# Kernel optimization log

Hardware: AMD Instinct MI355X
Metric: run time of the kernel (lower is better)

Reference implementation:

```python
import jax, jax.numpy as jnp
import numpy as np

DIM = 256
NUM_HEADS = 4
HEAD_DIM = DIM // NUM_HEADS
WINDOW_SIZES = [2, 4, 8, 16]
SCALE = HEAD_DIM ** -0.5


def setup_inputs() -> dict:
    key = jax.random.key(0)
    k1, k2, k3, k4 = jax.random.split(key, 4)
    B, C, H, W = 8, DIM, 128, 128
    x = jax.random.normal(k1, (B, C, H, W), dtype=jnp.float32)
    # 1x1 conv weights stored as [out, in]
    qkv_w = jax.random.normal(k2, (3 * DIM, DIM), dtype=jnp.float32) * (DIM ** -0.5)
    proj_w = jax.random.normal(k3, (DIM, DIM), dtype=jnp.float32) * (DIM ** -0.5)
    proj_b = jax.random.normal(k4, (DIM,), dtype=jnp.float32) * 0.01
    return {"x": x, "qkv_w": qkv_w, "proj_w": proj_w, "proj_b": proj_b}


def _window_attn(q, k, v, ws):
    # q,k,v: [B, H, W, hd] for one head; windowed self-attention of size ws
    B, H, W, hd = q.shape
    hg, wg = H // ws, W // ws

    def part(t):
        # [B,H,W,hd] -> [B, hg*wg, ws*ws, hd]
        t = t.reshape(B, hg, ws, wg, ws, hd).transpose(0, 1, 3, 2, 4, 5)
        return t.reshape(B, hg * wg, ws * ws, hd)

    qw, kw, vw = part(q), part(k), part(v)
    attn = jnp.einsum('bgqd,bgkd->bgqk', qw, kw) * SCALE
    attn = jax.nn.softmax(attn, axis=-1)
    out = jnp.einsum('bgqk,bgkd->bgqd', attn, vw)
    # reassemble: [B, hg, wg, ws, ws, hd] -> [B, H, W, hd]
    out = out.reshape(B, hg, wg, ws, ws, hd).transpose(0, 1, 3, 2, 4, 5)
    return out.reshape(B, H, W, hd)


def reference(x, qkv_w, proj_w, proj_b):
    B, C, H, W = x.shape
    # 1x1 conv qkv: [B, 3*dim, H, W] -> [3, B, nh, H, W, hd]
    qkv = jnp.einsum('bchw,oc->bohw', x, qkv_w)
    qkv = qkv.reshape(B, 3, NUM_HEADS, HEAD_DIM, H, W).transpose(1, 0, 2, 4, 5, 3)
    q, k, v = qkv[0], qkv[1], qkv[2]
    outs = []
    for i, ws in enumerate(WINDOW_SIZES):
        outs.append(_window_attn(q[:, i], k[:, i], v[:, i], ws))
    y = jnp.concatenate(outs, axis=-1)  # [B, H, W, dim]
    y = jnp.einsum('bhwc,oc->bhwo', y, proj_w) + proj_b
    y = y.transpose(0, 3, 1, 2)  # [B, dim, H, W]
    return y + x
```

## Files before the change

### kernel.cpp

```cpp
#include <hip/hip_runtime.h>
#include <hip/hip_bf16.h>
#include <cstddef>
#include <cstdint>

typedef unsigned short u16;
typedef unsigned int uint32;
typedef __attribute__((ext_vector_type(8))) short bf16x8;
typedef __attribute__((ext_vector_type(4))) float f32x4;

#define SPATIAL 16384
#define TOTAL_M 131072

__device__ __forceinline__ u16 f2b(float f) {
  __hip_bfloat16 h = __float2bfloat16(f);
  return *reinterpret_cast<u16*>(&h);
}
__device__ __forceinline__ uint32 pk2(float a, float b) {
  return (uint32)f2b(a) | ((uint32)f2b(b) << 16);
}
__device__ __forceinline__ float blo(uint32 u) {
  union { uint32 u; float f; } c; c.u = u << 16; return c.f;
}
__device__ __forceinline__ float bhi(uint32 u) {
  union { uint32 u; float f; } c; c.u = u & 0xffff0000u; return c.f;
}

__device__ __forceinline__ void gload_lds16(const u16* g, u16* l) {
  __builtin_amdgcn_global_load_lds(
      (const __attribute__((address_space(1))) void*)g,
      (__attribute__((address_space(3))) void*)l, 16, 0, 0);
}

template <int WS>
__device__ __forceinline__ size_t tok_base(int gw, int tt) {
  constexpr int WG = 128 / WS;
  constexpr int NWIN = WG * WG;
  int bb = gw / NWIN, rr = gw % NWIN;
  int gy = rr / WG, gx = rr % WG;
  int yy = gy * WS + tt / WS, xx = gx * WS + tt % WS;
  return (((size_t)bb * 128 + yy) * 128 + xx) * 768;
}

__global__ __launch_bounds__(256) void prep(const float* __restrict__ x,
                                            const float* __restrict__ qw,
                                            const float* __restrict__ pw,
                                            u16* __restrict__ xT,
                                            u16* __restrict__ wq,
                                            u16* __restrict__ wp) {
  const int tid = threadIdx.x;
  const int bid = blockIdx.x;
  if (bid >= 2048) {
    const int t = (bid - 2048) * 256 + tid;
#pragma unroll
    for (int i = 0; i < 16; ++i) {
      const int e = i * 4096 + t;
      if (e < 49152) {
        float4 v = *(const float4*)&qw[(size_t)e * 4];
        ushort4 o;
        o.x = f2b(v.x); o.y = f2b(v.y); o.z = f2b(v.z); o.w = f2b(v.w);
        *(ushort4*)&wq[(size_t)e * 4] = o;
      } else {
        float4 v = *(const float4*)&pw[(size_t)(e - 49152) * 4];
        ushort4 o;
        o.x = f2b(v.x); o.y = f2b(v.y); o.z = f2b(v.z); o.w = f2b(v.w);
        *(ushort4*)&wp[(size_t)(e - 49152) * 4] = o;
      }
    }
    return;
  }
  __shared__ u16 Ts[64 * 256];
  const int b = bid >> 8;
  const int sp0 = (bid & 255) * 64;
#pragma unroll
  for (int it = 0; it < 16; ++it) {
    int e = it * 256 + tid;
    int k = e >> 4;
    int c4 = (e & 15) * 4;
    float4 v = *(const float4*)&x[(((size_t)(b * 256 + k)) << 14) + sp0 + c4];
    Ts[(c4 + 0) * 256 + (k ^ ((((c4 + 0)) & 31) << 3))] = f2b(v.x);
    Ts[(c4 + 1) * 256 + (k ^ ((((c4 + 1)) & 31) << 3))] = f2b(v.y);
    Ts[(c4 + 2) * 256 + (k ^ ((((c4 + 2)) & 31) << 3))] = f2b(v.z);
    Ts[(c4 + 3) * 256 + (k ^ ((((c4 + 3)) & 31) << 3))] = f2b(v.w);
  }
  __syncthreads();
#pragma unroll
  for (int it = 0; it < 8; ++it) {
    int e = it * 256 + tid;
    int sp = e >> 5;
    int kc = (e & 31) * 8;
    bf16x8 row = *(const bf16x8*)&Ts[sp * 256 + (kc ^ ((sp & 31) << 3))];
    *(bf16x8*)&xT[((size_t)(b * 16384 + sp0 + sp)) * 256 + kc] = row;
  }
}

__global__ __launch_bounds__(256) void gemm_qkv(const u16* __restrict__ xT,
                                                const u16* __restrict__ wq,
                                                u16* __restrict__ qkv) {
  __shared__ u16 As[128 * 64];
  __shared__ u16 Bs[128 * 64];
  const int tid = threadIdx.x;
  const int n0 = blockIdx.x * 128;
  const int m0 = blockIdx.y * 128;
  const int lane = tid & 63, w = tid >> 6;
  const int wr = w >> 1, wc = w & 1;
  const int fr = lane & 15, fk = lane >> 4;
  const int frx = (fr & 7) << 3;
  f32x4 acc[4][4] = {};
  for (int kt = 0; kt < 4; ++kt) {
    const int k0 = kt * 64;
#pragma unroll
    for (int it = 0; it < 4; ++it) {
      int e = it * 256 + tid;
      int row = e >> 3;
      int kcs = ((e & 7) * 8) ^ ((row & 7) << 3);
      u16* la = &As[(it * 256 + (tid & 192)) * 8];
      u16* lb = &Bs[(it * 256 + (tid & 192)) * 8];
      gload_lds16(&xT[((size_t)(m0 + row) << 8) + k0 + kcs], la);
      gload_lds16(&wq[((size_t)(n0 + row) << 8) + k0 + kcs], lb);
    }
    __syncthreads();
#pragma unroll
    for (int kk = 0; kk < 2; ++kk) {
      const int kb = (kk * 32 + fk * 8) ^ frx;
      bf16x8 af[4], bfr[4];
#pragma unroll
      for (int i = 0; i < 4; ++i) {
        af[i] = *(const bf16x8*)&As[(wr * 64 + i * 16 + fr) * 64 + kb];
        bfr[i] = *(const bf16x8*)&Bs[(wc * 64 + i * 16 + fr) * 64 + kb];
      }
#pragma unroll
      for (int i = 0; i < 4; ++i)
#pragma unroll
        for (int j = 0; j < 4; ++j)
          acc[i][j] = __builtin_amdgcn_mfma_f32_16x16x32_bf16(bfr[j], af[i], acc[i][j], 0, 0, 0);
    }
    __syncthreads();
  }
#pragma unroll
  for (int i = 0; i < 4; ++i) {
    const size_t row = (size_t)(m0 + wr * 64 + i * 16 + fr) * 768;
#pragma unroll
    for (int j = 0; j < 4; ++j) {
      uint2 p;
      p.x = pk2(acc[i][j][0], acc[i][j][1]);
      p.y = pk2(acc[i][j][2], acc[i][j][3]);
      *(uint2*)&qkv[row + n0 + wc * 64 + j * 16 + fk * 4] = p;
    }
  }
}

template <int WS>
__device__ __forceinline__ void win_attn_body(u16* __restrict__ qkv, int head,
                                              int bid, u16 (*Ks)[68], u16 (*Vs)[68]) {
  constexpr int T = WS * WS;
  constexpr int G = 256 / T;
  const int tid = threadIdx.x;
  const int gw0 = bid * G;
  const int qoff = head * 64;

#pragma unroll
  for (int i = 0; i < 16; ++i) {
    int e4 = i * 256 + tid;
    int tok = e4 >> 4;
    int d4 = (e4 & 15) * 4;
    size_t base = tok_base<WS>(gw0 + tok / T, tok % T);
    *(uint2*)&Ks[tok][d4] = *(const uint2*)&qkv[base + 256 + qoff + d4];
    *(uint2*)&Vs[tok][d4] = *(const uint2*)&qkv[base + 512 + qoff + d4];
  }
  __syncthreads();

  const int myw = tid / T;
  const int mytt = tid % T;
  const size_t mybase = tok_base<WS>(gw0 + myw, mytt);

  float q[64];
#pragma unroll
  for (int d4 = 0; d4 < 16; ++d4) {
    uint2 q2 = *(const uint2*)&qkv[mybase + qoff + d4 * 4];
    q[d4 * 4 + 0] = blo(q2.x); q[d4 * 4 + 1] = bhi(q2.x);
    q[d4 * 4 + 2] = blo(q2.y); q[d4 * 4 + 3] = bhi(q2.y);
  }
  const int rbase = myw * T;

  float mmax = -1e30f, lsum = 0.f;
  for (int j = 0; j < T; ++j) {
    float s = 0.f;
#pragma unroll
    for (int d4 = 0; d4 < 16; ++d4) {
      uint2 k2 = *(const uint2*)&Ks[rbase + j][d4 * 4];
      s = fmaf(q[d4 * 4 + 0], blo(k2.x), s);
      s = fmaf(q[d4 * 4 + 1], bhi(k2.x), s);
      s = fmaf(q[d4 * 4 + 2], blo(k2.y), s);
      s = fmaf(q[d4 * 4 + 3], bhi(k2.y), s);
    }
    s *= 0.125f;
    const float mn = fmaxf(mmax, s);
    lsum = lsum * __expf(mmax - mn) + __expf(s - mn);
    mmax = mn;
  }
  const float inv = 1.f / lsum;

  float acc[64] = {};
  for (int j = 0; j < T; ++j) {
    float s = 0.f;
#pragma unroll
    for (int d4 = 0; d4 < 16; ++d4) {
      uint2 k2 = *(const uint2*)&Ks[rbase + j][d4 * 4];
      s = fmaf(q[d4 * 4 + 0], blo(k2.x), s);
      s = fmaf(q[d4 * 4 + 1], bhi(k2.x), s);
      s = fmaf(q[d4 * 4 + 2], blo(k2.y), s);
      s = fmaf(q[d4 * 4 + 3], bhi(k2.y), s);
    }
    const float p = __expf(s * 0.125f - mmax) * inv;
#pragma unroll
    for (int d4 = 0; d4 < 16; ++d4) {
      uint2 v2 = *(const uint2*)&Vs[rbase + j][d4 * 4];
      acc[d4 * 4 + 0] = fmaf(p, blo(v2.x), acc[d4 * 4 + 0]);
      acc[d4 * 4 + 1] = fmaf(p, bhi(v2.x), acc[d4 * 4 + 1]);
      acc[d4 * 4 + 2] = fmaf(p, blo(v2.y), acc[d4 * 4 + 2]);
      acc[d4 * 4 + 3] = fmaf(p, bhi(v2.y), acc[d4 * 4 + 3]);
    }
  }
#pragma unroll
  for (int d4 = 0; d4 < 16; ++d4) {
    uint2 o2;
    o2.x = pk2(acc[d4 * 4 + 0], acc[d4 * 4 + 1]);
    o2.y = pk2(acc[d4 * 4 + 2], acc[d4 * 4 + 3]);
    *(uint2*)&qkv[mybase + qoff + d4 * 4] = o2;
  }
}

template <int WS, int NW>
__device__ __forceinline__ void win_mfma_body(u16* __restrict__ qkv, int head,
                                              int bid, u16* __restrict__ smem) {
  constexpr int T = WS * WS;
  constexpr int G = 256 / T;
  constexpr int KT = T / 16;
  constexpr int KS = T / 32;
  constexpr int PL = T + 8;
  constexpr int NT = NW * 64;
  constexpr int QPW = (G * T / 16) / NW;
  u16* Ks = smem;
  u16* Vt = smem + 256 * 72;
  u16* Plds = Vt + 64 * 264;
  const int tid = threadIdx.x;
  const int gw0 = bid * G;
  const int qoff = head * 64;

#pragma unroll
  for (int it = 0; it < 4096 / NT; ++it) {
    int e = it * NT + tid;
    int tok = e >> 4;
    int d4 = (e & 15) * 4;
    int win = tok / T, tt = tok % T;
    size_t base = tok_base<WS>(gw0 + win, tt);
    uint2 kk = *(const uint2*)&qkv[base + 256 + qoff + d4];
    uint2 vv = *(const uint2*)&qkv[base + 512 + qoff + d4];
    *(uint2*)&Ks[tok * 72 + d4] = kk;
    Vt[(d4 + 0) * 264 + tok] = (u16)(vv.x & 0xffffu);
    Vt[(d4 + 1) * 264 + tok] = (u16)(vv.x >> 16);
    Vt[(d4 + 2) * 264 + tok] = (u16)(vv.y & 0xffffu);
    Vt[(d4 + 3) * 264 + tok] = (u16)(vv.y >> 16);
  }
  __syncthreads();

  const int w = tid >> 6, lane = tid & 63;
  const int fr = lane & 15, fk = lane >> 4;
  u16* prow = &Plds[(w * 16 + fr) * PL];

  for (int qi = 0; qi < QPW; ++qi) {
    const int qg = w * QPW + qi;
    const int win = qg / (T / 16);
    const int qt = qg % (T / 16);
    const int gw = gw0 + win;

    const size_t qb = tok_base<WS>(gw, qt * 16 + fr) + qoff;
    bf16x8 qf[2];
#pragma unroll
    for (int ds = 0; ds < 2; ++ds)
      qf[ds] = *(const bf16x8*)&qkv[qb + ds * 32 + fk * 8];

    f32x4 sv[KT];
#pragma unroll
    for (int kt = 0; kt < KT; ++kt) {
      const u16* krow = &Ks[(win * T + kt * 16 + fr) * 72];
      bf16x8 k0 = *(const bf16x8*)&krow[fk * 8];
      bf16x8 k1 = *(const bf16x8*)&krow[32 + fk * 8];
      f32x4 s = {};
      s = __builtin_amdgcn_mfma_f32_16x16x32_bf16(k0, qf[0], s, 0, 0, 0);
      s = __builtin_amdgcn_mfma_f32_16x16x32_bf16(k1, qf[1], s, 0, 0, 0);
      sv[kt] = s;
    }

    float rmax = -3e38f;
#pragma unroll
    for (int kt = 0; kt < KT; ++kt)
#pragma unroll
      for (int r = 0; r < 4; ++r) rmax = fmaxf(rmax, sv[kt][r]);
    rmax = fmaxf(rmax, __shfl_xor(rmax, 16));
    rmax = fmaxf(rmax, __shfl_xor(rmax, 32));
    const float m = rmax * 0.125f;
    float l = 0.f;
#pragma unroll
    for (int kt = 0; kt < KT; ++kt)
#pragma unroll
      for (int r = 0; r < 4; ++r) {
        float ev = __expf(sv[kt][r] * 0.125f - m);
        sv[kt][r] = ev;
        l += ev;
      }
    l += __shfl_xor(l, 16);
    l += __shfl_xor(l, 32);
    const float linv = 1.f / l;

#pragma unroll
    for (int kt = 0; kt < KT; ++kt) {
      uint2 pp;
      pp.x = pk2(sv[kt][0], sv[kt][1]);
      pp.y = pk2(sv[kt][2], sv[kt][3]);
      *(uint2*)&prow[kt * 16 + fk * 4] = pp;
    }
    __asm__ __volatile__("s_waitcnt lgkmcnt(0)" ::: "memory");
    __builtin_amdgcn_sched_barrier(0);

    f32x4 ov[4] = {};
#pragma unroll
    for (int ks = 0; ks < KS; ++ks) {
      bf16x8 pf = *(const bf16x8*)&prow[ks * 32 + fk * 8];
#pragma unroll
      for (int dt = 0; dt < 4; ++dt) {
        bf16x8 vf = *(const bf16x8*)&Vt[(dt * 16 + fr) * 264 + win * T + ks * 32 + fk * 8];
        ov[dt] = __builtin_amdgcn_mfma_f32_16x16x32_bf16(pf, vf, ov[dt], 0, 0, 0);
      }
    }

#pragma unroll
    for (int r = 0; r < 4; ++r) {
      float lr = __shfl(linv, fk * 4 + r);
      size_t ob = tok_base<WS>(gw, qt * 16 + fk * 4 + r) + qoff;
#pragma unroll
      for (int dt = 0; dt < 4; ++dt)
        qkv[ob + dt * 16 + fr] = f2b(ov[dt][r] * lr);
    }
  }
}

__global__ __launch_bounds__(256) void attn_a(u16* __restrict__ qkv) {
  __shared__ u16 smem[39936];
  const int bid = blockIdx.x;
  if (bid < 1024) {
    u16 (*Ks)[68] = (u16(*)[68])smem;
    u16 (*Vs)[68] = (u16(*)[68])(smem + 256 * 68);
    if (bid < 512)
      win_attn_body<2>(qkv, 0, bid, Ks, Vs);
    else
      win_attn_body<4>(qkv, 1, bid - 512, Ks, Vs);
  } else {
    win_mfma_body<8, 4>(qkv, 2, bid - 1024, smem);
  }
}

__global__ __launch_bounds__(512) void attn16(u16* __restrict__ qkv) {
  __shared__ u16 smem[256 * 72 + 64 * 264 + 8 * 16 * 264];
  win_mfma_body<16, 8>(qkv, 3, blockIdx.x, smem);
}

__global__ __launch_bounds__(256) void gemm_proj(const u16* __restrict__ qkv,
                                                 const u16* __restrict__ wp,
                                                 const float* __restrict__ bias,
                                                 const float* __restrict__ x,
                                                 float* __restrict__ out) {
  __shared__ u16 As[2][128 * 64];
  __shared__ u16 Bs[2][128 * 64];
  const int tid = threadIdx.x;
  const int bid = blockIdx.x;
  const int logical = (bid & 7) * 256 + (bid >> 3);
  const int m0 = (logical >> 1) * 128;
  const int n0 = (logical & 1) * 128;
  const int lane = tid & 63, w = tid >> 6;
  const int wr = w >> 1, wc = w & 1;
  const int fr = lane & 15, fk = lane >> 4;
  const int frx = (fr & 7) << 3;
  const int kcs = ((tid & 7) * 8) ^ (((tid >> 3) & 7) << 3);
  const int srow = tid >> 3;
  const int b = m0 >> 14;
  f32x4 acc[4][4] = {};

#define STAGE_PRJ(B, KT)                                                     \
  do {                                                                       \
    const int k0s = (KT)*64;                                                 \
    _Pragma("unroll") for (int it = 0; it < 4; ++it) {                       \
      int row = it * 32 + srow;                                              \
      u16* la = &As[B][(it * 256 + (tid & 192)) * 8];                        \
      u16* lb = &Bs[B][(it * 256 + (tid & 192)) * 8];                        \
      gload_lds16(&qkv[(size_t)(m0 + row) * 768 + k0s + kcs], la);           \
      gload_lds16(&wp[((size_t)(n0 + row) << 8) + k0s + kcs], lb);           \
    }                                                                        \
  } while (0)

#define COMP_PRJ(B)                                                          \
  do {                                                                       \
    _Pragma("unroll") for (int kk = 0; kk < 2; ++kk) {                       \
      const int kb = (kk * 32 + fk * 8) ^ frx;                               \
      bf16x8 af[4], bfr[4];                                                  \
      _Pragma("unroll") for (int i = 0; i < 4; ++i) {                        \
        af[i] = *(const bf16x8*)&As[B][(wr * 64 + i * 16 + fr) * 64 + kb];   \
        bfr[i] = *(const bf16x8*)&Bs[B][(wc * 64 + i * 16 + fr) * 64 + kb];  \
      }                                                                      \
      _Pragma("unroll") for (int i = 0; i < 4; ++i)                          \
          _Pragma("unroll") for (int j = 0; j < 4; ++j) acc[i][j] =          \
          __builtin_amdgcn_mfma_f32_16x16x32_bf16(af[i], bfr[j],             \
                                                  acc[i][j], 0, 0, 0);       \
    }                                                                        \
  } while (0)

#define PHASE(WAITN)                                                         \
  asm volatile("s_waitcnt vmcnt(" #WAITN ")" ::: "memory");                  \
  __builtin_amdgcn_s_barrier();                                              \
  __builtin_amdgcn_sched_barrier(0)

#define PHASE_END()                                                          \
  __builtin_amdgcn_sched_barrier(0);                                         \
  __builtin_amdgcn_s_barrier()

  STAGE_PRJ(0, 0);
  STAGE_PRJ(1, 1);
  PHASE(8);
  COMP_PRJ(0);
  PHASE_END();
  STAGE_PRJ(0, 2);
  PHASE(8);
  COMP_PRJ(1);
  PHASE_END();
  STAGE_PRJ(1, 3);
  PHASE(8);
  COMP_PRJ(0);
  PHASE_END();
  PHASE(0);
  COMP_PRJ(1);
#undef STAGE_PRJ
#undef COMP_PRJ
#undef PHASE
#undef PHASE_END

#pragma unroll
  for (int i = 0; i < 4; ++i) {
    const int sp = (m0 & 16383) + wr * 64 + i * 16 + fk * 4;
#pragma unroll
    for (int j = 0; j < 4; ++j) {
      const int n = n0 + wc * 64 + j * 16 + fr;
      const size_t o = ((size_t)(b * 256 + n) << 14) + sp;
      const float4 r4 = *(const float4*)&x[o];
      const float bb = bias[n];
      float4 v = make_float4(acc[i][j][0] + bb + r4.x, acc[i][j][1] + bb + r4.y,
                             acc[i][j][2] + bb + r4.z, acc[i][j][3] + bb + r4.w);
      *(float4*)&out[o] = v;
    }
  }
}

extern "C" void kernel_launch(void* const* d_in, const int* in_sizes, int n_in,
                              void* d_out, int out_size, void* d_ws, size_t ws_size,
                              hipStream_t stream) {
  const float* x = (const float*)d_in[0];
  const float* qkv_w = (const float*)d_in[1];
  const float* proj_w = (const float*)d_in[2];
  const float* proj_b = (const float*)d_in[3];
  float* out = (float*)d_out;
  u16* qkv = (u16*)d_ws;
  u16* xT = qkv + (size_t)131072 * 768;
  u16* wq = xT + (size_t)131072 * 256;
  u16* wp = wq + (size_t)768 * 256;

  prep<<<2064, 256, 0, stream>>>(x, qkv_w, proj_w, xT, wq, wp);
  gemm_qkv<<<dim3(6, 1024), 256, 0, stream>>>(xT, wq, qkv);
  attn_a<<<1536, 256, 0, stream>>>(qkv);
  attn16<<<512, 512, 0, stream>>>(qkv);
  gemm_proj<<<2048, 256, 0, stream>>>(qkv, wp, proj_b, x, out);
}
```

Measured before the change: 302.9 us.

## Merge all window-attention heads into one 512-thread launch; cache scores in scalar path

Both attention kernels become a single 512-thread kernel that dispatches the four heads by block index, which removes one launch and lets the heads run concurrently. The scalar small-window path now keeps all QK scores in a register array and computes the softmax in two passes, so it no longer recomputes the dot products. The ws=8 MFMA path handles twice as many windows per block with a parameterized V-transpose pitch. The shared-memory footprint grows to about 155 KB per block, which limits occupancy to one block per CU. The fully unrolled score arrays also raise register pressure.

Measured after the change: 294.9 us. 1.03x faster.

```diff
diff --git a/kernel.cpp b/kernel.cpp
--- a/kernel.cpp
+++ b/kernel.cpp
@@ -149,18 +149,20 @@
   }
 }
 
-template <int WS>
+template <int WS, int NT>
 __device__ __forceinline__ void win_attn_body(u16* __restrict__ qkv, int head,
-                                              int bid, u16 (*Ks)[68], u16 (*Vs)[68]) {
+                                              int bid, u16* __restrict__ smem) {
   constexpr int T = WS * WS;
-  constexpr int G = 256 / T;
+  constexpr int G = NT / T;
+  u16 (*Ks)[68] = (u16(*)[68])smem;
+  u16 (*Vs)[68] = (u16(*)[68])(smem + NT * 68);
   const int tid = threadIdx.x;
   const int gw0 = bid * G;
   const int qoff = head * 64;
 
 #pragma unroll
   for (int i = 0; i < 16; ++i) {
-    int e4 = i * 256 + tid;
+    int e4 = i * NT + tid;
     int tok = e4 >> 4;
     int d4 = (e4 & 15) * 4;
     size_t base = tok_base<WS>(gw0 + tok / T, tok % T);
@@ -182,7 +184,9 @@
   }
   const int rbase = myw * T;
 
-  float mmax = -1e30f, lsum = 0.f;
+  float sarr[T];
+  float mmax = -1e30f;
+#pragma unroll
   for (int j = 0; j < T; ++j) {
     float s = 0.f;
 #pragma unroll
@@ -193,25 +197,21 @@
       s = fmaf(q[d4 * 4 + 2], blo(k2.y), s);
       s = fmaf(q[d4 * 4 + 3], bhi(k2.y), s);
     }
-    s *= 0.125f;
-    const float mn = fmaxf(mmax, s);
-    lsum = lsum * __expf(mmax - mn) + __expf(s - mn);
-    mmax = mn;
+    sarr[j] = s * 0.125f;
+    mmax = fmaxf(mmax, sarr[j]);
+  }
+  float lsum = 0.f;
+#pragma unroll
+  for (int j = 0; j < T; ++j) {
+    sarr[j] = __expf(sarr[j] - mmax);
+    lsum += sarr[j];
   }
   const float inv = 1.f / lsum;
 
   float acc[64] = {};
+#pragma unroll
   for (int j = 0; j < T; ++j) {
-    float s = 0.f;
-#pragma unroll
-    for (int d4 = 0; d4 < 16; ++d4) {
-      uint2 k2 = *(const uint2*)&Ks[rbase + j][d4 * 4];
-      s = fmaf(q[d4 * 4 + 0], blo(k2.x), s);
-      s = fmaf(q[d4 * 4 + 1], bhi(k2.x), s);
-      s = fmaf(q[d4 * 4 + 2], blo(k2.y), s);
-      s = fmaf(q[d4 * 4 + 3], bhi(k2.y), s);
-    }
-    const float p = __expf(s * 0.125f - mmax) * inv;
+    const float p = sarr[j] * inv;
 #pragma unroll
     for (int d4 = 0; d4 < 16; ++d4) {
       uint2 v2 = *(const uint2*)&Vs[rbase + j][d4 * 4];
@@ -230,25 +230,26 @@
   }
 }
 
-template <int WS, int NW>
+template <int WS, int NW, int G>
 __device__ __forceinline__ void win_mfma_body(u16* __restrict__ qkv, int head,
                                               int bid, u16* __restrict__ smem) {
   constexpr int T = WS * WS;
-  constexpr int G = 256 / T;
+  constexpr int TOK = G * T;
   constexpr int KT = T / 16;
   constexpr int KS = T / 32;
   constexpr int PL = T + 8;
+  constexpr int VP = TOK + 8;
   constexpr int NT = NW * 64;
   constexpr int QPW = (G * T / 16) / NW;
   u16* Ks = smem;
-  u16* Vt = smem + 256 * 72;
-  u16* Plds = Vt + 64 * 264;
+  u16* Vt = smem + TOK * 72;
+  u16* Plds = Vt + 64 * VP;
   const int tid = threadIdx.x;
   const int gw0 = bid * G;
   const int qoff = head * 64;
 
 #pragma unroll
-  for (int it = 0; it < 4096 / NT; ++it) {
+  for (int it = 0; it < TOK * 16 / NT; ++it) {
     int e = it * NT + tid;
     int tok = e >> 4;
     int d4 = (e & 15) * 4;
@@ -257,10 +258,10 @@
     uint2 kk = *(const uint2*)&qkv[base + 256 + qoff + d4];
     uint2 vv = *(const uint2*)&qkv[base + 512 + qoff + d4];
     *(uint2*)&Ks[tok * 72 + d4] = kk;
-    Vt[(d4 + 0) * 264 + tok] = (u16)(vv.x & 0xffffu);
-    Vt[(d4 + 1) * 264 + tok] = (u16)(vv.x >> 16);
-    Vt[(d4 + 2) * 264 + tok] = (u16)(vv.y & 0xffffu);
-    Vt[(d4 + 3) * 264 + tok] = (u16)(vv.y >> 16);
+    Vt[(d4 + 0) * VP + tok] = (u16)(vv.x & 0xffffu);
+    Vt[(d4 + 1) * VP + tok] = (u16)(vv.x >> 16);
+    Vt[(d4 + 2) * VP + tok] = (u16)(vv.y & 0xffffu);
+    Vt[(d4 + 3) * VP + tok] = (u16)(vv.y >> 16);
   }
   __syncthreads();
 
@@ -329,7 +330,7 @@
       bf16x8 pf = *(const bf16x8*)&prow[ks * 32 + fk * 8];
 #pragma unroll
       for (int dt = 0; dt < 4; ++dt) {
-        bf16x8 vf = *(const bf16x8*)&Vt[(dt * 16 + fr) * 264 + win * T + ks * 32 + fk * 8];
+        bf16x8 vf = *(const bf16x8*)&Vt[(dt * 16 + fr) * VP + win * T + ks * 32 + fk * 8];
         ov[dt] = __builtin_amdgcn_mfma_f32_16x16x32_bf16(pf, vf, ov[dt], 0, 0, 0);
       }
     }
@@ -345,24 +346,17 @@
   }
 }
 
-__global__ __launch_bounds__(256) void attn_a(u16* __restrict__ qkv) {
-  __shared__ u16 smem[39936];
+__global__ __launch_bounds__(512) void attn_all(u16* __restrict__ qkv) {
+  __shared__ u16 smem[79360];
   const int bid = blockIdx.x;
-  if (bid < 1024) {
-    u16 (*Ks)[68] = (u16(*)[68])smem;
-    u16 (*Vs)[68] = (u16(*)[68])(smem + 256 * 68);
-    if (bid < 512)
-      win_attn_body<2>(qkv, 0, bid, Ks, Vs);
-    else
-      win_attn_body<4>(qkv, 1, bid - 512, Ks, Vs);
-  } else {
-    win_mfma_body<8, 4>(qkv, 2, bid - 1024, smem);
-  }
-}
-
-__global__ __launch_bounds__(512) void attn16(u16* __restrict__ qkv) {
-  __shared__ u16 smem[256 * 72 + 64 * 264 + 8 * 16 * 264];
-  win_mfma_body<16, 8>(qkv, 3, blockIdx.x, smem);
+  if (bid < 256)
+    win_attn_body<2, 512>(qkv, 0, bid, smem);
+  else if (bid < 512)
+    win_attn_body<4, 512>(qkv, 1, bid - 256, smem);
+  else if (bid < 768)
+    win_mfma_body<8, 8, 8>(qkv, 2, bid - 512, smem);
+  else
+    win_mfma_body<16, 8, 1>(qkv, 3, bid - 768, smem);
 }
 
 __global__ __launch_bounds__(256) void gemm_proj(const u16* __restrict__ qkv,
@@ -474,7 +468,6 @@
 
   prep<<<2064, 256, 0, stream>>>(x, qkv_w, proj_w, xT, wq, wp);
   gemm_qkv<<<dim3(6, 1024), 256, 0, stream>>>(xT, wq, qkv);
-  attn_a<<<1536, 256, 0, stream>>>(qkv);
-  attn16<<<512, 512, 0, stream>>>(qkv);
+  attn_all<<<1280, 512, 0, stream>>>(qkv);
   gemm_proj<<<2048, 256, 0, stream>>>(qkv, wp, proj_b, x, out);
 }
```
